# Kernel optimization log

Hardware: AMD Instinct MI355X
Metric: run time of the kernel (lower is better)

Reference implementation:

```python
import jax, jax.numpy as jnp
import numpy as np

NMS_SIGMA = 2.0
MASK_THRESH = 0.5
N = 500
H = W = 256
NUM_CLS = 80


def setup_inputs() -> dict:
    key = jax.random.key(0)
    k1, k2, k3 = jax.random.split(key, 3)
    mask_preds = jax.random.uniform(k1, (N, H, W), dtype=jnp.float32)
    cate_scores = jax.random.uniform(k2, (N,), dtype=jnp.float32)
    cate_labels = jax.random.randint(k3, (N,), 0, NUM_CLS, dtype=jnp.int32)
    return {"mask_preds": mask_preds, "cate_scores": cate_scores, "cate_labels": cate_labels}


def reference(mask_preds, cate_scores, cate_labels):
    n = mask_preds.shape[0]
    # binarize masks (SOLOv2 inference: seg_masks = seg_preds > mask_thresh)
    seg_masks = (mask_preds > MASK_THRESH).astype(mask_preds.dtype)  # [N,H,W]
    sum_masks = seg_masks.sum(axis=(1, 2))                           # [N]
    # mask scoring: average soft score inside the binary mask
    seg_scores = (mask_preds * seg_masks).sum(axis=(1, 2)) / jnp.maximum(sum_masks, 1.0)
    scores = cate_scores * seg_scores                                # [N]
    # sort descending by score (matrix-NMS assumes sorted order)
    order = jnp.argsort(-scores)
    scores = scores[order]
    labels = cate_labels[order]
    flat = seg_masks[order].reshape(n, -1)                           # [N,HW]
    sums = sum_masks[order]
    # pairwise mask IoU, upper-triangular (j suppressed by i<j)
    inter = flat @ flat.T                                            # [N,N]
    union = sums[:, None] + sums[None, :] - inter
    iou = jnp.triu(inter / jnp.maximum(union, 1.0), k=1)
    label_match = jnp.triu((labels[:, None] == labels[None, :]).astype(iou.dtype), k=1)
    decay_iou = iou * label_match                                    # [N,N]
    # gaussian matrix-NMS decay
    compensate_iou = decay_iou.max(axis=0)                           # [N]
    decay_matrix = jnp.exp(-NMS_SIGMA * (decay_iou ** 2 - compensate_iou[:, None] ** 2))
    coeff = decay_matrix.min(axis=0)                                 # [N]
    updated_scores = scores * coeff
    return updated_scores
```

## Files before the change

### kernel.cpp

```cpp
#include <hip/hip_runtime.h>
#include <cstdint>

typedef unsigned long long u64;

#define THRESH 0.5f
#define SIGMA 2.0f
#define TPB 64
#define NSPLIT 16
#define CST 66

__device__ __forceinline__ bool better(float sa, int a, float sb, int b) {
    return (sa > sb) || (sa == sb && a < b);
}

__global__ __launch_bounds__(512) void k_pack(
    const float* __restrict__ preds, const float* __restrict__ cate,
    u64* __restrict__ packed, float* __restrict__ score, float* __restrict__ sum,
    int HW)
{
    const int i = blockIdx.x;
    const float* src = preds + (size_t)i * HW;
    u64* dst = packed + (size_t)i * (HW >> 6);
    const int tid = threadIdx.x;
    const int wave = tid >> 6, lane = tid & 63;
    double ssum = 0.0;
    int cnt = 0;
    const int iters = HW >> 11;
    for (int k = 0; k < iters; ++k) {
        const int p = (k << 11) + (wave << 8) + (lane << 2);
        const float4 v = *reinterpret_cast<const float4*>(src + p);
        const bool b0 = v.x > THRESH, b1 = v.y > THRESH, b2 = v.z > THRESH, b3 = v.w > THRESH;
        const u64 m0 = __ballot(b0);
        const u64 m1 = __ballot(b1);
        const u64 m2 = __ballot(b2);
        const u64 m3 = __ballot(b3);
        if (lane < 4) {
            const u64 m = (lane == 0) ? m0 : (lane == 1) ? m1 : (lane == 2) ? m2 : m3;
            dst[(k << 5) + (wave << 2) + lane] = m;
        }
        cnt += (int)b0 + (int)b1 + (int)b2 + (int)b3;
        ssum += (b0 ? (double)v.x : 0.0) + (b1 ? (double)v.y : 0.0)
              + (b2 ? (double)v.z : 0.0) + (b3 ? (double)v.w : 0.0);
    }
    for (int off = 32; off > 0; off >>= 1) {
        ssum += __shfl_down(ssum, off);
        cnt  += __shfl_down(cnt, off);
    }
    __shared__ double ls[8];
    __shared__ int lc[8];
    if (lane == 0) { ls[wave] = ssum; lc[wave] = cnt; }
    __syncthreads();
    if (tid == 0) {
        double S = 0.0; int C = 0;
        #pragma unroll
        for (int w = 0; w < 8; ++w) { S += ls[w]; C += lc[w]; }
        score[i] = cate[i] * (float)(S / (double)(C > 1 ? C : 1));
        sum[i] = (float)C;
    }
}

__global__ __launch_bounds__(256) void k_inter(
    const u64* __restrict__ packed, unsigned* __restrict__ part,
    int N, int WORDS, int NT)
{
    __shared__ __align__(16) u64 sm[2 * TPB][CST];
    int b = blockIdx.x;
    int ti = 0, rowlen = NT;
    while (b >= rowlen) { b -= rowlen; ++ti; --rowlen; }
    const int tj = ti + b;
    const int kwords = WORDS / NSPLIT;
    const int kbase = blockIdx.y * kwords;

    const int tid = threadIdx.x;
    const int a = tid >> 4, bb = tid & 15;

    const int half = kwords >> 1;
    for (int idx = tid; idx < 2 * TPB * half; idx += 256) {
        const int ml = idx / half;
        const int w = (idx - ml * half) << 1;
        const int g = (ml < TPB) ? (ti * TPB + ml) : (tj * TPB + (ml - TPB));
        u64 x0 = 0, x1 = 0;
        if (g < N) {
            const u64* p = packed + (size_t)g * WORDS + kbase + w;
            x0 = p[0];
            x1 = p[1];
        }
        sm[ml][w] = x0;
        sm[ml][w + 1] = x1;
    }
    __syncthreads();

    unsigned acc[4][4] = {};
    #pragma unroll 4
    for (int w = 0; w < kwords; w += 2) {
        u64 pi0[4], pi1[4], pj0[4], pj1[4];
        #pragma unroll
        for (int t = 0; t < 4; ++t) {
            const ulonglong2 q = *reinterpret_cast<const ulonglong2*>(&sm[4 * a + t][w]);
            pi0[t] = q.x; pi1[t] = q.y;
        }
        #pragma unroll
        for (int s = 0; s < 4; ++s) {
            const ulonglong2 q = *reinterpret_cast<const ulonglong2*>(&sm[TPB + bb + 16 * s][w]);
            pj0[s] = q.x; pj1[s] = q.y;
        }
        #pragma unroll
        for (int t = 0; t < 4; ++t)
            #pragma unroll
            for (int s = 0; s < 4; ++s)
                acc[t][s] += (unsigned)__popcll(pi0[t] & pj0[s])
                           + (unsigned)__popcll(pi1[t] & pj1[s]);
    }
    #pragma unroll
    for (int t = 0; t < 4; ++t)
        #pragma unroll
        for (int s = 0; s < 4; ++s) {
            const int gi = ti * TPB + 4 * a + t;
            const int gj = tj * TPB + bb + 16 * s;
            if (gj < N && gi < gj)
                part[((size_t)gi * N + gj) * NSPLIT + blockIdx.y] = acc[t][s];
        }
}

__device__ __forceinline__ unsigned fold16(const unsigned* __restrict__ p) {
    const uint4* q = reinterpret_cast<const uint4*>(p);
    unsigned s = 0;
    #pragma unroll
    for (int k = 0; k < 4; ++k) {
        const uint4 v = q[k];
        s += v.x + v.y + v.z + v.w;
    }
    return s;
}

__global__ __launch_bounds__(256) void k_comp(
    const unsigned* __restrict__ part, const float* __restrict__ score,
    const float* __restrict__ sum, const int* __restrict__ labels,
    float* __restrict__ comp, int N)
{
    const int bI = blockIdx.x;
    const float sb = score[bI], sub = sum[bI];
    const int lb = labels[bI];
    const int tid = threadIdx.x;
    float m = 0.0f;
    for (int a = tid; a < N; a += 256) {
        if (a == bI || labels[a] != lb) continue;
        const float sa = score[a];
        if (!better(sa, a, sb, bI)) continue;
        const int lo = a < bI ? a : bI, hi = a < bI ? bI : a;
        const float inter = (float)fold16(part + ((size_t)lo * N + hi) * NSPLIT);
        const float un = sum[a] + sub - inter;
        m = fmaxf(m, inter / fmaxf(un, 1.0f));
    }
    for (int off = 32; off > 0; off >>= 1) m = fmaxf(m, __shfl_down(m, off));
    __shared__ float lm[4];
    const int wave = tid >> 6, lane = tid & 63;
    if (lane == 0) lm[wave] = m;
    __syncthreads();
    if (tid == 0) comp[bI] = fmaxf(fmaxf(lm[0], lm[1]), fmaxf(lm[2], lm[3]));
}

__global__ __launch_bounds__(256) void k_final(
    const unsigned* __restrict__ part, const float* __restrict__ score,
    const float* __restrict__ sum, const int* __restrict__ labels,
    const float* __restrict__ comp, float* __restrict__ out, int N)
{
    const int bI = blockIdx.x;
    const float sb = score[bI], sub = sum[bI];
    const int lb = labels[bI];
    const int tid = threadIdx.x;
    float m = -3.0e38f;
    int r = 0;
    for (int a = tid; a < N; a += 256) {
        const float sa = score[a];
        const bool bet = (a != bI) && better(sa, a, sb, bI);
        r += (int)bet;
        float d = 0.0f;
        if (bet && labels[a] == lb) {
            const int lo = a < bI ? a : bI, hi = a < bI ? bI : a;
            const float inter = (float)fold16(part + ((size_t)lo * N + hi) * NSPLIT);
            const float un = sum[a] + sub - inter;
            d = inter / fmaxf(un, 1.0f);
        }
        const float ca = comp[a];
        m = fmaxf(m, d * d - ca * ca);
    }
    for (int off = 32; off > 0; off >>= 1) {
        m = fmaxf(m, __shfl_down(m, off));
        r += __shfl_down(r, off);
    }
    __shared__ float lm[4];
    __shared__ int lr[4];
    const int wave = tid >> 6, lane = tid & 63;
    if (lane == 0) { lm[wave] = m; lr[wave] = r; }
    __syncthreads();
    if (tid == 0) {
        const float mm = fmaxf(fmaxf(lm[0], lm[1]), fmaxf(lm[2], lm[3]));
        const int rank = lr[0] + lr[1] + lr[2] + lr[3];
        out[rank] = sb * expf(-SIGMA * mm);
    }
}

extern "C" void kernel_launch(void* const* d_in, const int* in_sizes, int n_in,
                              void* d_out, int out_size, void* d_ws, size_t ws_size,
                              hipStream_t stream)
{
    const float* preds  = (const float*)d_in[0];
    const float* cate   = (const float*)d_in[1];
    const int*   labels = (const int*)d_in[2];
    float* out = (float*)d_out;

    const int N = in_sizes[1];
    const int HW = in_sizes[0] / N;
    const int WORDS = HW >> 6;

    char* ws = (char*)d_ws;
    size_t off = 0;
    auto take = [&](size_t bytes) -> void* {
        void* p = ws + off;
        off = (off + bytes + 255) & ~(size_t)255;
        return p;
    };
    u64*      packed = (u64*)     take((size_t)N * WORDS * sizeof(u64));
    float*    score  = (float*)   take((size_t)N * sizeof(float));
    float*    sum    = (float*)   take((size_t)N * sizeof(float));
    float*    comp   = (float*)   take((size_t)N * sizeof(float));
    unsigned* part   = (unsigned*)take((size_t)N * N * NSPLIT * sizeof(unsigned));
    (void)ws_size; (void)n_in; (void)out_size;

    k_pack<<<N, 512, 0, stream>>>(preds, cate, packed, score, sum, HW);

    const int NT = (N + TPB - 1) / TPB;
    dim3 grid(NT * (NT + 1) / 2, NSPLIT);
    k_inter<<<grid, 256, 0, stream>>>(packed, part, N, WORDS, NT);

    k_comp<<<N, 256, 0, stream>>>(part, score, sum, labels, comp, N);

    k_final<<<N, 256, 0, stream>>>(part, score, sum, labels, comp, out, N);
}
```

Baseline: 245.5 us.

## Split mask packing into quarter-mask blocks and finalize scores in shared memory

The packing kernel now launches four 256-thread blocks per mask instead of one 512-thread block, and each thread issues four float4 loads per iteration to raise memory-level parallelism. Each block writes partial sums and counts. Every block of the comp and final kernels then combines those partials into scores and sums and stages score, sum and label arrays in shared memory. This removes the serial per-mask reduction from packing, at the cost of each later block recomputing all N scores.

```diff
diff --git a/kernel.cpp b/kernel.cpp
--- a/kernel.cpp
+++ b/kernel.cpp
@@ -8,54 +8,60 @@
 #define TPB 64
 #define NSPLIT 16
 #define CST 66
+#define MAXN 512
 
 __device__ __forceinline__ bool better(float sa, int a, float sb, int b) {
     return (sa > sb) || (sa == sb && a < b);
 }
 
-__global__ __launch_bounds__(512) void k_pack(
-    const float* __restrict__ preds, const float* __restrict__ cate,
-    u64* __restrict__ packed, float* __restrict__ score, float* __restrict__ sum,
-    int HW)
-{
-    const int i = blockIdx.x;
-    const float* src = preds + (size_t)i * HW;
-    u64* dst = packed + (size_t)i * (HW >> 6);
+__global__ __launch_bounds__(256) void k_pack(
+    const float* __restrict__ preds, u64* __restrict__ packed,
+    double* __restrict__ pssum, int* __restrict__ pcnt, int HW)
+{
+    const int task = blockIdx.x;
+    const int i = task >> 2, sub = task & 3;
+    const int seg = HW >> 2;
+    const float* src = preds + (size_t)i * HW + (size_t)sub * seg;
+    u64* dst = packed + (size_t)i * (HW >> 6) + (size_t)sub * (seg >> 6);
     const int tid = threadIdx.x;
     const int wave = tid >> 6, lane = tid & 63;
     double ssum = 0.0;
     int cnt = 0;
-    const int iters = HW >> 11;
+    const int iters = seg >> 12;
     for (int k = 0; k < iters; ++k) {
-        const int p = (k << 11) + (wave << 8) + (lane << 2);
-        const float4 v = *reinterpret_cast<const float4*>(src + p);
-        const bool b0 = v.x > THRESH, b1 = v.y > THRESH, b2 = v.z > THRESH, b3 = v.w > THRESH;
-        const u64 m0 = __ballot(b0);
-        const u64 m1 = __ballot(b1);
-        const u64 m2 = __ballot(b2);
-        const u64 m3 = __ballot(b3);
-        if (lane < 4) {
-            const u64 m = (lane == 0) ? m0 : (lane == 1) ? m1 : (lane == 2) ? m2 : m3;
-            dst[(k << 5) + (wave << 2) + lane] = m;
-        }
-        cnt += (int)b0 + (int)b1 + (int)b2 + (int)b3;
-        ssum += (b0 ? (double)v.x : 0.0) + (b1 ? (double)v.y : 0.0)
-              + (b2 ? (double)v.z : 0.0) + (b3 ? (double)v.w : 0.0);
+        const int base = (k << 12) + (wave << 10) + (lane << 2);
+        const float4 v0 = *reinterpret_cast<const float4*>(src + base);
+        const float4 v1 = *reinterpret_cast<const float4*>(src + base + 256);
+        const float4 v2 = *reinterpret_cast<const float4*>(src + base + 512);
+        const float4 v3 = *reinterpret_cast<const float4*>(src + base + 768);
+        #pragma unroll
+        for (int q = 0; q < 4; ++q) {
+            const float4 v = (q == 0) ? v0 : (q == 1) ? v1 : (q == 2) ? v2 : v3;
+            const bool b0 = v.x > THRESH, b1 = v.y > THRESH, b2 = v.z > THRESH, b3 = v.w > THRESH;
+            const u64 m0 = __ballot(b0);
+            const u64 m1 = __ballot(b1);
+            const u64 m2 = __ballot(b2);
+            const u64 m3 = __ballot(b3);
+            if (lane < 4) {
+                const u64 m = (lane == 0) ? m0 : (lane == 1) ? m1 : (lane == 2) ? m2 : m3;
+                dst[(k << 6) + (wave << 4) + (q << 2) + lane] = m;
+            }
+            cnt += (int)b0 + (int)b1 + (int)b2 + (int)b3;
+            ssum += (b0 ? (double)v.x : 0.0) + (b1 ? (double)v.y : 0.0)
+                  + (b2 ? (double)v.z : 0.0) + (b3 ? (double)v.w : 0.0);
+        }
     }
     for (int off = 32; off > 0; off >>= 1) {
         ssum += __shfl_down(ssum, off);
         cnt  += __shfl_down(cnt, off);
     }
-    __shared__ double ls[8];
-    __shared__ int lc[8];
+    __shared__ double ls[4];
+    __shared__ int lc[4];
     if (lane == 0) { ls[wave] = ssum; lc[wave] = cnt; }
     __syncthreads();
     if (tid == 0) {
-        double S = 0.0; int C = 0;
-        #pragma unroll
-        for (int w = 0; w < 8; ++w) { S += ls[w]; C += lc[w]; }
-        score[i] = cate[i] * (float)(S / (double)(C > 1 ? C : 1));
-        sum[i] = (float)C;
+        pssum[task] = ls[0] + ls[1] + ls[2] + ls[3];
+        pcnt[task]  = lc[0] + lc[1] + lc[2] + lc[3];
     }
 }
 
@@ -133,23 +139,43 @@
     return s;
 }
 
+__device__ __forceinline__ void finalize_scores(
+    const double* __restrict__ pssum, const int* __restrict__ pcnt,
+    const float* __restrict__ cate, const int* __restrict__ labels,
+    float* s_score, float* s_sum, int* s_label, int N, int tid)
+{
+    for (int idx = tid; idx < N; idx += 256) {
+        const double S = ((pssum[4*idx] + pssum[4*idx+1]) + pssum[4*idx+2]) + pssum[4*idx+3];
+        const int C = ((pcnt[4*idx] + pcnt[4*idx+1]) + pcnt[4*idx+2]) + pcnt[4*idx+3];
+        s_score[idx] = cate[idx] * (float)(S / (double)(C > 1 ? C : 1));
+        s_sum[idx] = (float)C;
+        s_label[idx] = labels[idx];
+    }
+    __syncthreads();
+}
+
 __global__ __launch_bounds__(256) void k_comp(
-    const unsigned* __restrict__ part, const float* __restrict__ score,
-    const float* __restrict__ sum, const int* __restrict__ labels,
+    const unsigned* __restrict__ part,
+    const double* __restrict__ pssum, const int* __restrict__ pcnt,
+    const float* __restrict__ cate, const int* __restrict__ labels,
     float* __restrict__ comp, int N)
 {
+    __shared__ float s_score[MAXN];
+    __shared__ float s_sum[MAXN];
+    __shared__ int s_label[MAXN];
+    const int tid = threadIdx.x;
+    finalize_scores(pssum, pcnt, cate, labels, s_score, s_sum, s_label, N, tid);
+
     const int bI = blockIdx.x;
-    const float sb = score[bI], sub = sum[bI];
-    const int lb = labels[bI];
-    const int tid = threadIdx.x;
+    const float sb = s_score[bI], sub = s_sum[bI];
+    const int lb = s_label[bI];
     float m = 0.0f;
     for (int a = tid; a < N; a += 256) {
-        if (a == bI || labels[a] != lb) continue;
-        const float sa = score[a];
-        if (!better(sa, a, sb, bI)) continue;
+        if (a == bI || s_label[a] != lb) continue;
+        if (!better(s_score[a], a, sb, bI)) continue;
         const int lo = a < bI ? a : bI, hi = a < bI ? bI : a;
         const float inter = (float)fold16(part + ((size_t)lo * N + hi) * NSPLIT);
-        const float un = sum[a] + sub - inter;
+        const float un = s_sum[a] + sub - inter;
         m = fmaxf(m, inter / fmaxf(un, 1.0f));
     }
     for (int off = 32; off > 0; off >>= 1) m = fmaxf(m, __shfl_down(m, off));
@@ -161,25 +187,30 @@
 }
 
 __global__ __launch_bounds__(256) void k_final(
-    const unsigned* __restrict__ part, const float* __restrict__ score,
-    const float* __restrict__ sum, const int* __restrict__ labels,
+    const unsigned* __restrict__ part,
+    const double* __restrict__ pssum, const int* __restrict__ pcnt,
+    const float* __restrict__ cate, const int* __restrict__ labels,
     const float* __restrict__ comp, float* __restrict__ out, int N)
 {
+    __shared__ float s_score[MAXN];
+    __shared__ float s_sum[MAXN];
+    __shared__ int s_label[MAXN];
+    const int tid = threadIdx.x;
+    finalize_scores(pssum, pcnt, cate, labels, s_score, s_sum, s_label, N, tid);
+
     const int bI = blockIdx.x;
-    const float sb = score[bI], sub = sum[bI];
-    const int lb = labels[bI];
-    const int tid = threadIdx.x;
+    const float sb = s_score[bI], sub = s_sum[bI];
+    const int lb = s_label[bI];
     float m = -3.0e38f;
     int r = 0;
     for (int a = tid; a < N; a += 256) {
-        const float sa = score[a];
-        const bool bet = (a != bI) && better(sa, a, sb, bI);
+        const bool bet = (a != bI) && better(s_score[a], a, sb, bI);
         r += (int)bet;
         float d = 0.0f;
-        if (bet && labels[a] == lb) {
+        if (bet && s_label[a] == lb) {
             const int lo = a < bI ? a : bI, hi = a < bI ? bI : a;
             const float inter = (float)fold16(part + ((size_t)lo * N + hi) * NSPLIT);
-            const float un = sum[a] + sub - inter;
+            const float un = s_sum[a] + sub - inter;
             d = inter / fmaxf(un, 1.0f);
         }
         const float ca = comp[a];
@@ -222,19 +253,19 @@
         return p;
     };
     u64*      packed = (u64*)     take((size_t)N * WORDS * sizeof(u64));
-    float*    score  = (float*)   take((size_t)N * sizeof(float));
-    float*    sum    = (float*)   take((size_t)N * sizeof(float));
+    double*   pssum  = (double*)  take((size_t)N * 4 * sizeof(double));
+    int*      pcnt   = (int*)     take((size_t)N * 4 * sizeof(int));
     float*    comp   = (float*)   take((size_t)N * sizeof(float));
     unsigned* part   = (unsigned*)take((size_t)N * N * NSPLIT * sizeof(unsigned));
     (void)ws_size; (void)n_in; (void)out_size;
 
-    k_pack<<<N, 512, 0, stream>>>(preds, cate, packed, score, sum, HW);
+    k_pack<<<N * 4, 256, 0, stream>>>(preds, packed, pssum, pcnt, HW);
 
     const int NT = (N + TPB - 1) / TPB;
     dim3 grid(NT * (NT + 1) / 2, NSPLIT);
     k_inter<<<grid, 256, 0, stream>>>(packed, part, N, WORDS, NT);
 
-    k_comp<<<N, 256, 0, stream>>>(part, score, sum, labels, comp, N);
-
-    k_final<<<N, 256, 0, stream>>>(part, score, sum, labels, comp, out, N);
-}
+    k_comp<<<N, 256, 0, stream>>>(part, pssum, pcnt, cate, labels, comp, N);
+
+    k_final<<<N, 256, 0, stream>>>(part, pssum, pcnt, cate, labels, comp, out, N);
+}
```

Result: no change. 244.1 us (-0.6%).
